# Kernel tuning notes

Hardware: AMD Instinct MI355X
Metric: run time of the kernel (lower is better)

Reference implementation:

```python
import jax, jax.numpy as jnp
import numpy as np

EPS = 1e-7
ROUTING_ITERS = 3

def squash(s, axis=-1):
    # v = (|s|^2 / (1+|s|^2)) * s / |s|
    sq = jnp.sum(jnp.square(s), axis=axis, keepdims=True)
    return (sq / (1.0 + sq)) * s / jnp.sqrt(sq + EPS)

def setup_inputs() -> dict:
    key = jax.random.key(0)
    k1, k2 = jax.random.split(key)
    B, NI, DI = 64, 2048, 8      # batch, input capsules, input capsule dim
    NC, DC = 32, 16              # output capsules, output capsule dim
    x = jax.random.normal(k1, (B, NI, DI), dtype=jnp.float32)
    W = jax.random.normal(k2, (NC, NI, DC, DI), dtype=jnp.float32) * 0.05
    return {"x": x, "W": W}

def reference(x, W):
    # x: [B, NI, DI], W: [NC, NI, DC, DI]
    # tf.einsum('iabc,abdc->iabd') == project each input capsule per output capsule
    u = jnp.einsum('bif,cidf->bcid', x, W)          # [B, NC, NI, DC]
    B, NC, NI, DC = u.shape
    b = jnp.zeros((B, NC, NI, 1), dtype=u.dtype)
    v = None
    for _ in range(ROUTING_ITERS):
        c = jax.nn.softmax(b, axis=1)                # coupling over output capsules
        s = jnp.sum(c * u, axis=2, keepdims=True)    # [B, NC, 1, DC]
        v = squash(s, axis=-1)                       # [B, NC, 1, DC]
        # original: reduce_sum(matmul(u, tile(v)^T), axis=3) == NI * <u_i, v>
        agree = jnp.sum(u * v, axis=-1, keepdims=True)  # [B, NC, NI, 1]
        b = b + NI * agree
    return jnp.squeeze(v, axis=2)                    # [B, NC, DC]
```

## Files before the change

kernel.cpp:

```cpp
#include <hip/hip_runtime.h>

#define NI 2048
#define NB 64
#define NC 32
#define DC 16
#define DI 8

static constexpr float SQ_EPS = 1e-7f;

typedef float f8 __attribute__((ext_vector_type(8)));

template <int MODE>
__global__
__attribute__((amdgpu_flat_work_group_size(256, 256), amdgpu_waves_per_eu(2, 2)))
void route_pass(
    const float* __restrict__ x, const float* __restrict__ W,
    const float* __restrict__ veff, float* __restrict__ partial)
{
    __shared__ float4 wbuf[2][2048];
    __shared__ float4 xbuf[512];

    const int tid   = threadIdx.x;
    const int wave  = tid >> 6;
    const int lane  = tid & 63;
    const int c     = lane & 31;
    const int dg    = lane >> 5;
    const int brel0 = wave * 4;
    const int b0    = blockIdx.y * 16 + brel0;
    const int i0    = blockIdx.x * 16;

    const float4* Wf4 = reinterpret_cast<const float4*>(W);

    f8 s0 = {}, s1 = {}, s2 = {}, s3 = {};

    f8 va = {}, vb = {}, vc = {}, vd = {};
    if (MODE == 1) {
        va = *reinterpret_cast<const f8*>(veff + (((size_t)(b0+0)*2 + dg)*32 + c)*8);
        vb = *reinterpret_cast<const f8*>(veff + (((size_t)(b0+1)*2 + dg)*32 + c)*8);
        vc = *reinterpret_cast<const f8*>(veff + (((size_t)(b0+2)*2 + dg)*32 + c)*8);
        vd = *reinterpret_cast<const f8*>(veff + (((size_t)(b0+3)*2 + dg)*32 + c)*8);
    }

#define STAGE_ASYNC(buf, itile)                                              \
    {                                                                        \
        _Pragma("unroll")                                                    \
        for (int o = 0; o < 8; ++o) {                                        \
            const int s  = o * 256 + wave * 64 + lane;                       \
            const int q  = s >> 5;                                           \
            const int cc = ((s & 31) - q) & 31;                              \
            const int il = q >> 5;                                           \
            const int k  = ((q >> 1) & 15) + ((q & 1) << 4);                 \
            const float4* srcp = Wf4 + ((size_t)cc * NI + (itile) + il) * 32 + k; \
            __builtin_amdgcn_global_load_lds(                                \
                (const __attribute__((address_space(1))) void*)srcp,         \
                (__attribute__((address_space(3))) void*)&wbuf[buf][o * 256 + wave * 64], \
                16, 0, 0);                                                   \
        }                                                                    \
    }

    STAGE_ASYNC(0, i0);
    {
        const float4* xg = reinterpret_cast<const float4*>(x);
        const int t0 = tid, t1 = tid + 256;
        xbuf[t0] = xg[((size_t)(blockIdx.y*16 + (t0>>5)) * NI + i0 + ((t0&31)>>1))*2 + (t0&1)];
        xbuf[t1] = xg[((size_t)(blockIdx.y*16 + (t1>>5)) * NI + i0 + ((t1&31)>>1))*2 + (t1&1)];
    }
    __syncthreads();

    int cur = 0;
    for (int rnd = 0; rnd < 8; ++rnd) {
        if (rnd < 7) STAGE_ASYNC(cur ^ 1, i0 + (rnd + 1) * 2);

        const float4* wb = wbuf[cur];

#pragma unroll
        for (int il = 0; il < 2; ++il) {
            const int iloc = rnd * 2 + il;
            const float4 xa0 = xbuf[(brel0+0)*32 + iloc*2], xa1 = xbuf[(brel0+0)*32 + iloc*2+1];
            const float4 xb0 = xbuf[(brel0+1)*32 + iloc*2], xb1 = xbuf[(brel0+1)*32 + iloc*2+1];
            const float4 xc0 = xbuf[(brel0+2)*32 + iloc*2], xc1 = xbuf[(brel0+2)*32 + iloc*2+1];
            const float4 xd0 = xbuf[(brel0+3)*32 + iloc*2], xd1 = xbuf[(brel0+3)*32 + iloc*2+1];

            f8 u0 = {}, u1 = {}, u2 = {}, u3 = {};
#pragma unroll
            for (int dd = 0; dd < 8; ++dd) {
                const int ql = (il * 16 + dd * 2) * 2 + dg;
                const int qh = ql + 2;
                const float4 wl = wb[ql * 32 + ((c + ql) & 31)];
                const float4 wh = wb[qh * 32 + ((c + qh) & 31)];
                u0[dd] = wl.x*xa0.x + wl.y*xa0.y + wl.z*xa0.z + wl.w*xa0.w
                       + wh.x*xa1.x + wh.y*xa1.y + wh.z*xa1.z + wh.w*xa1.w;
                u1[dd] = wl.x*xb0.x + wl.y*xb0.y + wl.z*xb0.z + wl.w*xb0.w
                       + wh.x*xb1.x + wh.y*xb1.y + wh.z*xb1.z + wh.w*xb1.w;
                u2[dd] = wl.x*xc0.x + wl.y*xc0.y + wl.z*xc0.z + wl.w*xc0.w
                       + wh.x*xc1.x + wh.y*xc1.y + wh.z*xc1.z + wh.w*xc1.w;
                u3[dd] = wl.x*xd0.x + wl.y*xd0.y + wl.z*xd0.z + wl.w*xd0.w
                       + wh.x*xd1.x + wh.y*xd1.y + wh.z*xd1.z + wh.w*xd1.w;
            }

            if (MODE == 0) {
                const float cu = 1.0f / 32.0f;
                s0 += u0 * cu; s1 += u1 * cu; s2 += u2 * cu; s3 += u3 * cu;
            } else {
#pragma unroll
                for (int pr = 0; pr < 2; ++pr) {
                    const f8& ue = pr ? u2 : u0;
                    const f8& uo = pr ? u3 : u1;
                    const f8& ve = pr ? vc : va;
                    const f8& vo = pr ? vd : vb;
                    float pe = 0.0f, po = 0.0f;
#pragma unroll
                    for (int kk = 0; kk < 8; ++kk) {
                        pe += ue[kk] * ve[kk];
                        po += uo[kk] * vo[kk];
                    }
                    const float send = (dg == 0) ? po : pe;
                    const float recv = __shfl_xor(send, 32);
                    float a = ((dg == 0) ? pe : po) + recv;
                    float m = a;
#pragma unroll
                    for (int off = 16; off >= 1; off >>= 1)
                        m = fmaxf(m, __shfl_xor(m, off));
                    const float e = __expf(a - m);
                    float t = e;
#pragma unroll
                    for (int off = 16; off >= 1; off >>= 1)
                        t += __shfl_xor(t, off);
                    const float mine  = e / t;
                    const float other = __shfl_xor(mine, 32);
                    const float ce = (dg == 0) ? mine : other;
                    const float co = (dg == 0) ? other : mine;
                    if (pr == 0) { s0 += u0 * ce; s1 += u1 * co; }
                    else         { s2 += u2 * ce; s3 += u3 * co; }
                }
            }
        }

        __syncthreads();
        cur ^= 1;
    }
#undef STAGE_ASYNC

    {
        const int pblk = blockIdx.y * gridDim.x + blockIdx.x;
        float* gp = partial +
            (((size_t)pblk * 16 + brel0) * 128 + dg * 64 + c * 2) * 4;
        *reinterpret_cast<f8*>(gp)        = s0;
        *reinterpret_cast<f8*>(gp +  512) = s1;
        *reinterpret_cast<f8*>(gp + 1024) = s2;
        *reinterpret_cast<f8*>(gp + 1536) = s3;
    }
}

__global__ __launch_bounds__(512) void reduce_squash(
    const float* __restrict__ partial, float* __restrict__ veff,
    float* __restrict__ out, int phase)
{
    __shared__ float4 red[512];
    const int b   = blockIdx.x;
    const int sub = threadIdx.x & 127;
    const int ibq = threadIdx.x >> 7;
    const int c   = (sub >> 2) & 31;
    const int dq  = sub & 3;

    const float* base = partial
        + ((size_t)(b >> 4) * 2048 + (b & 15)) * 512
        + (dq >> 1) * 256 + c * 8 + (dq & 1) * 4
        + (size_t)ibq * 32 * 8192;
    float4 acc = make_float4(0.f, 0.f, 0.f, 0.f);
#pragma unroll 8
    for (int ib = 0; ib < 32; ++ib) {
        const float4 p = *reinterpret_cast<const float4*>(base + (size_t)ib * 8192);
        acc.x += p.x; acc.y += p.y; acc.z += p.z; acc.w += p.w;
    }
    red[threadIdx.x] = acc;
    __syncthreads();
    if (threadIdx.x < 128) {
        const float4 a1 = red[sub + 128];
        const float4 a2 = red[sub + 256];
        const float4 a3 = red[sub + 384];
        acc.x += a1.x + a2.x + a3.x;
        acc.y += a1.y + a2.y + a3.y;
        acc.z += a1.z + a2.z + a3.z;
        acc.w += a1.w + a2.w + a3.w;

        float sq = acc.x*acc.x + acc.y*acc.y + acc.z*acc.z + acc.w*acc.w;
        sq += __shfl_xor(sq, 1);
        sq += __shfl_xor(sq, 2);
        const float scale = sq / ((1.0f + sq) * sqrtf(sq + SQ_EPS));

        if (phase == 3) {
            float4* op = reinterpret_cast<float4*>(out + ((size_t)b * NC + c) * DC + dq * 4);
            *op = make_float4(scale*acc.x, scale*acc.y, scale*acc.z, scale*acc.w);
        } else {
            const float ns = scale * (float)NI;
            float4* vp = reinterpret_cast<float4*>(
                veff + (((size_t)b * 2 + (dq >> 1)) * 32 + c) * 8 + (dq & 1) * 4);
            if (phase == 1) {
                *vp = make_float4(ns*acc.x, ns*acc.y, ns*acc.z, ns*acc.w);
            } else {
                float4 old = *vp;
                *vp = make_float4(old.x + ns*acc.x, old.y + ns*acc.y,
                                  old.z + ns*acc.z, old.w + ns*acc.w);
            }
        }
    }
}

extern "C" void kernel_launch(void* const* d_in, const int* in_sizes, int n_in,
                              void* d_out, int out_size, void* d_ws, size_t ws_size,
                              hipStream_t stream) {
    (void)in_sizes; (void)n_in; (void)out_size; (void)ws_size;
    const float* x = (const float*)d_in[0];
    const float* W = (const float*)d_in[1];

    float* partial = (float*)d_ws;
    float* veff    = (float*)d_out;

    const dim3 grid(128, 4);

    route_pass<0><<<grid, 256, 0, stream>>>(x, W, nullptr, partial);
    reduce_squash<<<64, 512, 0, stream>>>(partial, veff, nullptr, 1);

    route_pass<1><<<grid, 256, 0, stream>>>(x, W, veff, partial);
    reduce_squash<<<64, 512, 0, stream>>>(partial, veff, nullptr, 2);

    route_pass<1><<<grid, 256, 0, stream>>>(x, W, veff, partial);
    reduce_squash<<<64, 512, 0, stream>>>(partial, nullptr, (float*)d_out, 3);
}
```

Before: 195.5 us.

## Halve LDS stage size and double i-tile grid for higher occupancy

```diff
diff --git a/kernel.cpp b/kernel.cpp
--- a/kernel.cpp
+++ b/kernel.cpp
@@ -10,15 +10,15 @@
 
 typedef float f8 __attribute__((ext_vector_type(8)));
 
-template <int MODE>
+template <int MODE, int NIB>
 __global__
-__attribute__((amdgpu_flat_work_group_size(256, 256), amdgpu_waves_per_eu(2, 2)))
+__attribute__((amdgpu_flat_work_group_size(256, 256), amdgpu_waves_per_eu(2, 8)))
 void route_pass(
     const float* __restrict__ x, const float* __restrict__ W,
     const float* __restrict__ veff, float* __restrict__ partial)
 {
-    __shared__ float4 wbuf[2][2048];
-    __shared__ float4 xbuf[512];
+    __shared__ float4 wbuf[2][1024];
+    __shared__ float4 xbuf[32 * NIB];
 
     const int tid   = threadIdx.x;
     const int wave  = tid >> 6;
@@ -27,7 +27,7 @@
     const int dg    = lane >> 5;
     const int brel0 = wave * 4;
     const int b0    = blockIdx.y * 16 + brel0;
-    const int i0    = blockIdx.x * 16;
+    const int i0    = blockIdx.x * NIB;
 
     const float4* Wf4 = reinterpret_cast<const float4*>(W);
 
@@ -41,16 +41,14 @@
         vd = *reinterpret_cast<const f8*>(veff + (((size_t)(b0+3)*2 + dg)*32 + c)*8);
     }
 
-#define STAGE_ASYNC(buf, itile)                                              \
+#define STAGE_ASYNC(buf, it)                                                 \
     {                                                                        \
         _Pragma("unroll")                                                    \
-        for (int o = 0; o < 8; ++o) {                                        \
+        for (int o = 0; o < 4; ++o) {                                        \
             const int s  = o * 256 + wave * 64 + lane;                       \
             const int q  = s >> 5;                                           \
             const int cc = ((s & 31) - q) & 31;                              \
-            const int il = q >> 5;                                           \
-            const int k  = ((q >> 1) & 15) + ((q & 1) << 4);                 \
-            const float4* srcp = Wf4 + ((size_t)cc * NI + (itile) + il) * 32 + k; \
+            const float4* srcp = Wf4 + ((size_t)cc * NI + (it)) * 32 + q;    \
             __builtin_amdgcn_global_load_lds(                                \
                 (const __attribute__((address_space(1))) void*)srcp,         \
                 (__attribute__((address_space(3))) void*)&wbuf[buf][o * 256 + wave * 64], \
@@ -61,78 +59,76 @@
     STAGE_ASYNC(0, i0);
     {
         const float4* xg = reinterpret_cast<const float4*>(x);
-        const int t0 = tid, t1 = tid + 256;
-        xbuf[t0] = xg[((size_t)(blockIdx.y*16 + (t0>>5)) * NI + i0 + ((t0&31)>>1))*2 + (t0&1)];
-        xbuf[t1] = xg[((size_t)(blockIdx.y*16 + (t1>>5)) * NI + i0 + ((t1&31)>>1))*2 + (t1&1)];
+#pragma unroll
+        for (int t = tid; t < 32 * NIB; t += 256) {
+            const int brel = t / (NIB * 2);
+            const int rem  = t % (NIB * 2);
+            xbuf[t] = xg[((size_t)(blockIdx.y * 16 + brel) * NI + i0 + (rem >> 1)) * 2 + (rem & 1)];
+        }
     }
     __syncthreads();
 
     int cur = 0;
-    for (int rnd = 0; rnd < 8; ++rnd) {
-        if (rnd < 7) STAGE_ASYNC(cur ^ 1, i0 + (rnd + 1) * 2);
+    for (int rnd = 0; rnd < NIB; ++rnd) {
+        if (rnd < NIB - 1) STAGE_ASYNC(cur ^ 1, i0 + rnd + 1);
 
         const float4* wb = wbuf[cur];
 
-#pragma unroll
-        for (int il = 0; il < 2; ++il) {
-            const int iloc = rnd * 2 + il;
-            const float4 xa0 = xbuf[(brel0+0)*32 + iloc*2], xa1 = xbuf[(brel0+0)*32 + iloc*2+1];
-            const float4 xb0 = xbuf[(brel0+1)*32 + iloc*2], xb1 = xbuf[(brel0+1)*32 + iloc*2+1];
-            const float4 xc0 = xbuf[(brel0+2)*32 + iloc*2], xc1 = xbuf[(brel0+2)*32 + iloc*2+1];
-            const float4 xd0 = xbuf[(brel0+3)*32 + iloc*2], xd1 = xbuf[(brel0+3)*32 + iloc*2+1];
-
-            f8 u0 = {}, u1 = {}, u2 = {}, u3 = {};
-#pragma unroll
-            for (int dd = 0; dd < 8; ++dd) {
-                const int ql = (il * 16 + dd * 2) * 2 + dg;
-                const int qh = ql + 2;
-                const float4 wl = wb[ql * 32 + ((c + ql) & 31)];
-                const float4 wh = wb[qh * 32 + ((c + qh) & 31)];
-                u0[dd] = wl.x*xa0.x + wl.y*xa0.y + wl.z*xa0.z + wl.w*xa0.w
-                       + wh.x*xa1.x + wh.y*xa1.y + wh.z*xa1.z + wh.w*xa1.w;
-                u1[dd] = wl.x*xb0.x + wl.y*xb0.y + wl.z*xb0.z + wl.w*xb0.w
-                       + wh.x*xb1.x + wh.y*xb1.y + wh.z*xb1.z + wh.w*xb1.w;
-                u2[dd] = wl.x*xc0.x + wl.y*xc0.y + wl.z*xc0.z + wl.w*xc0.w
-                       + wh.x*xc1.x + wh.y*xc1.y + wh.z*xc1.z + wh.w*xc1.w;
-                u3[dd] = wl.x*xd0.x + wl.y*xd0.y + wl.z*xd0.z + wl.w*xd0.w
-                       + wh.x*xd1.x + wh.y*xd1.y + wh.z*xd1.z + wh.w*xd1.w;
-            }
-
-            if (MODE == 0) {
-                const float cu = 1.0f / 32.0f;
-                s0 += u0 * cu; s1 += u1 * cu; s2 += u2 * cu; s3 += u3 * cu;
-            } else {
-#pragma unroll
-                for (int pr = 0; pr < 2; ++pr) {
-                    const f8& ue = pr ? u2 : u0;
-                    const f8& uo = pr ? u3 : u1;
-                    const f8& ve = pr ? vc : va;
-                    const f8& vo = pr ? vd : vb;
-                    float pe = 0.0f, po = 0.0f;
-#pragma unroll
-                    for (int kk = 0; kk < 8; ++kk) {
-                        pe += ue[kk] * ve[kk];
-                        po += uo[kk] * vo[kk];
-                    }
-                    const float send = (dg == 0) ? po : pe;
-                    const float recv = __shfl_xor(send, 32);
-                    float a = ((dg == 0) ? pe : po) + recv;
-                    float m = a;
-#pragma unroll
-                    for (int off = 16; off >= 1; off >>= 1)
-                        m = fmaxf(m, __shfl_xor(m, off));
-                    const float e = __expf(a - m);
-                    float t = e;
-#pragma unroll
-                    for (int off = 16; off >= 1; off >>= 1)
-                        t += __shfl_xor(t, off);
-                    const float mine  = e / t;
-                    const float other = __shfl_xor(mine, 32);
-                    const float ce = (dg == 0) ? mine : other;
-                    const float co = (dg == 0) ? other : mine;
-                    if (pr == 0) { s0 += u0 * ce; s1 += u1 * co; }
-                    else         { s2 += u2 * ce; s3 += u3 * co; }
+        const float4 xa0 = xbuf[(brel0+0)*(NIB*2) + rnd*2], xa1 = xbuf[(brel0+0)*(NIB*2) + rnd*2+1];
+        const float4 xb0 = xbuf[(brel0+1)*(NIB*2) + rnd*2], xb1 = xbuf[(brel0+1)*(NIB*2) + rnd*2+1];
+        const float4 xc0 = xbuf[(brel0+2)*(NIB*2) + rnd*2], xc1 = xbuf[(brel0+2)*(NIB*2) + rnd*2+1];
+        const float4 xd0 = xbuf[(brel0+3)*(NIB*2) + rnd*2], xd1 = xbuf[(brel0+3)*(NIB*2) + rnd*2+1];
+
+        f8 u0 = {}, u1 = {}, u2 = {}, u3 = {};
+#pragma unroll
+        for (int dd = 0; dd < 8; ++dd) {
+            const int q0 = (dg * 8 + dd) * 2;
+            const float4 wl = wb[ q0      * 32 + ((c + q0    ) & 31)];
+            const float4 wh = wb[(q0 + 1) * 32 + ((c + q0 + 1) & 31)];
+            u0[dd] = wl.x*xa0.x + wl.y*xa0.y + wl.z*xa0.z + wl.w*xa0.w
+                   + wh.x*xa1.x + wh.y*xa1.y + wh.z*xa1.z + wh.w*xa1.w;
+            u1[dd] = wl.x*xb0.x + wl.y*xb0.y + wl.z*xb0.z + wl.w*xb0.w
+                   + wh.x*xb1.x + wh.y*xb1.y + wh.z*xb1.z + wh.w*xb1.w;
+            u2[dd] = wl.x*xc0.x + wl.y*xc0.y + wl.z*xc0.z + wl.w*xc0.w
+                   + wh.x*xc1.x + wh.y*xc1.y + wh.z*xc1.z + wh.w*xc1.w;
+            u3[dd] = wl.x*xd0.x + wl.y*xd0.y + wl.z*xd0.z + wl.w*xd0.w
+                   + wh.x*xd1.x + wh.y*xd1.y + wh.z*xd1.z + wh.w*xd1.w;
+        }
+
+        if (MODE == 0) {
+            const float cu = 1.0f / 32.0f;
+            s0 += u0 * cu; s1 += u1 * cu; s2 += u2 * cu; s3 += u3 * cu;
+        } else {
+#pragma unroll
+            for (int pr = 0; pr < 2; ++pr) {
+                const f8& ue = pr ? u2 : u0;
+                const f8& uo = pr ? u3 : u1;
+                const f8& ve = pr ? vc : va;
+                const f8& vo = pr ? vd : vb;
+                float pe = 0.0f, po = 0.0f;
+#pragma unroll
+                for (int kk = 0; kk < 8; ++kk) {
+                    pe += ue[kk] * ve[kk];
+                    po += uo[kk] * vo[kk];
                 }
+                const float send = (dg == 0) ? po : pe;
+                const float recv = __shfl_xor(send, 32);
+                float a = ((dg == 0) ? pe : po) + recv;
+                float m = a;
+#pragma unroll
+                for (int off = 16; off >= 1; off >>= 1)
+                    m = fmaxf(m, __shfl_xor(m, off));
+                const float e = __expf(a - m);
+                float t = e;
+#pragma unroll
+                for (int off = 16; off >= 1; off >>= 1)
+                    t += __shfl_xor(t, off);
+                const float mine  = e / t;
+                const float other = __shfl_xor(mine, 32);
+                const float ce = (dg == 0) ? mine : other;
+                const float co = (dg == 0) ? other : mine;
+                if (pr == 0) { s0 += u0 * ce; s1 += u1 * co; }
+                else         { s2 += u2 * ce; s3 += u3 * co; }
             }
         }
 
@@ -152,6 +148,7 @@
     }
 }
 
+template <int SLABS>
 __global__ __launch_bounds__(512) void reduce_squash(
     const float* __restrict__ partial, float* __restrict__ veff,
     float* __restrict__ out, int phase)
@@ -164,12 +161,12 @@
     const int dq  = sub & 3;
 
     const float* base = partial
-        + ((size_t)(b >> 4) * 2048 + (b & 15)) * 512
+        + ((size_t)(b >> 4) * SLABS * 16 + (b & 15)) * 512
         + (dq >> 1) * 256 + c * 8 + (dq & 1) * 4
-        + (size_t)ibq * 32 * 8192;
+        + (size_t)ibq * (SLABS / 4) * 8192;
     float4 acc = make_float4(0.f, 0.f, 0.f, 0.f);
 #pragma unroll 8
-    for (int ib = 0; ib < 32; ++ib) {
+    for (int ib = 0; ib < SLABS / 4; ++ib) {
         const float4 p = *reinterpret_cast<const float4*>(base + (size_t)ib * 8192);
         acc.x += p.x; acc.y += p.y; acc.z += p.z; acc.w += p.w;
     }
@@ -210,21 +207,28 @@
 extern "C" void kernel_launch(void* const* d_in, const int* in_sizes, int n_in,
                               void* d_out, int out_size, void* d_ws, size_t ws_size,
                               hipStream_t stream) {
-    (void)in_sizes; (void)n_in; (void)out_size; (void)ws_size;
+    (void)in_sizes; (void)n_in; (void)out_size;
     const float* x = (const float*)d_in[0];
     const float* W = (const float*)d_in[1];
 
     float* partial = (float*)d_ws;
     float* veff    = (float*)d_out;
 
-    const dim3 grid(128, 4);
-
-    route_pass<0><<<grid, 256, 0, stream>>>(x, W, nullptr, partial);
-    reduce_squash<<<64, 512, 0, stream>>>(partial, veff, nullptr, 1);
-
-    route_pass<1><<<grid, 256, 0, stream>>>(x, W, veff, partial);
-    reduce_squash<<<64, 512, 0, stream>>>(partial, veff, nullptr, 2);
-
-    route_pass<1><<<grid, 256, 0, stream>>>(x, W, veff, partial);
-    reduce_squash<<<64, 512, 0, stream>>>(partial, nullptr, (float*)d_out, 3);
+    if (ws_size >= (size_t)1024 * 16 * 512 * 4) {
+        const dim3 grid(256, 4);
+        route_pass<0, 8><<<grid, 256, 0, stream>>>(x, W, nullptr, partial);
+        reduce_squash<256><<<64, 512, 0, stream>>>(partial, veff, nullptr, 1);
+        route_pass<1, 8><<<grid, 256, 0, stream>>>(x, W, veff, partial);
+        reduce_squash<256><<<64, 512, 0, stream>>>(partial, veff, nullptr, 2);
+        route_pass<1, 8><<<grid, 256, 0, stream>>>(x, W, veff, partial);
+        reduce_squash<256><<<64, 512, 0, stream>>>(partial, nullptr, (float*)d_out, 3);
+    } else {
+        const dim3 grid(128, 4);
+        route_pass<0, 16><<<grid, 256, 0, stream>>>(x, W, nullptr, partial);
+        reduce_squash<128><<<64, 512, 0, stream>>>(partial, veff, nullptr, 1);
+        route_pass<1, 16><<<grid, 256, 0, stream>>>(x, W, veff, partial);
+        reduce_squash<128><<<64, 512, 0, stream>>>(partial, veff, nullptr, 2);
+        route_pass<1, 16><<<grid, 256, 0, stream>>>(x, W, veff, partial);
+        reduce_squash<128><<<64, 512, 0, stream>>>(partial, nullptr, (float*)d_out, 3);
+    }
 }
```

After: 208.5 us. 6.6% more time.
